# Performance work log

Measured on AMD Instinct MI355X. Metric: run time of the kernel, lower is better.

The kernel has to match this reference:

```python
import jax, jax.numpy as jnp
import numpy as np

B, N, F_IN, F_OUT = 4, 512, 128, 128


def setup_inputs() -> dict:
    key = jax.random.key(0)
    k_x, k_adj, k_wm, k_wu = jax.random.split(key, 4)
    x = jax.random.normal(k_x, (B, N, F_IN), dtype=jnp.float32)
    # binary adjacency mask (dense), avg degree ~ 0.1*N
    adj = (jax.random.uniform(k_adj, (B, N, N)) < 0.1).astype(jnp.float32)
    # Linear weights stored as [in, out] (transpose of torch's [out, in])
    s_m = 1.0 / np.sqrt(2 * F_IN)
    s_u = 1.0 / np.sqrt(F_IN + F_OUT)
    W_msg = jax.random.uniform(k_wm, (2 * F_IN, F_OUT), minval=-s_m, maxval=s_m, dtype=jnp.float32)
    b_msg = jnp.zeros((F_OUT,), dtype=jnp.float32)
    W_upd = jax.random.uniform(k_wu, (F_IN + F_OUT, F_OUT), minval=-s_u, maxval=s_u, dtype=jnp.float32)
    b_upd = jnp.zeros((F_OUT,), dtype=jnp.float32)
    return {"x": x, "adj": adj, "W_msg": W_msg, "b_msg": b_msg,
            "W_upd": W_upd, "b_upd": b_upd}


def reference(x, adj, W_msg, b_msg, W_upd, b_upd):
    # Linear(cat(x_i, x_j)) == x_i @ W_i + x_j @ W_j + b  (exploit linearity to
    # avoid materializing the [B,N,N,2F] concat; math identical to torch module)
    F_in = x.shape[-1]
    Wi, Wj = W_msg[:F_in], W_msg[F_in:]
    xi = jnp.einsum('bnf,fo->bno', x, Wi)            # [B,N,out], i-term
    xj = jnp.einsum('bnf,fo->bno', x, Wj)            # [B,N,out], j-term
    # messages[b,i,j,:] = relu(xi[b,i] + xj[b,j] + b_msg); dropout is identity (eval)
    messages = jax.nn.relu(xi[:, :, None, :] + xj[:, None, :, :] + b_msg)
    # mask by adjacency and sum over j
    aggregated = jnp.einsum('bijo,bij->bio', messages, adj)  # [B,N,out]
    h_new = jnp.concatenate([x, aggregated], axis=-1)        # [B,N,F+out]
    out = jax.nn.relu(jnp.einsum('bnf,fo->bno', h_new, W_upd) + b_upd)
    return out
```

## Files before the change

kernel.cpp:

```cpp
#include <hip/hip_runtime.h>
#include <hip/hip_fp16.h>

constexpr int B_   = 4;
constexpr int N_   = 512;
constexpr int F    = 128;
constexpr int R1B  = 8;
constexpr int R2B  = 8;
constexpr int LSTW = 520;

__global__ __launch_bounds__(512, 2) void k_pre(
    const float* __restrict__ x,
    const float* __restrict__ adj,
    const float* __restrict__ Wmsg,
    const float* __restrict__ bmsg,
    const float* __restrict__ Wupd,
    float*  __restrict__ xi,
    __half* __restrict__ xjH,
    float*  __restrict__ xu,
    int*    __restrict__ lstG,
    int*    __restrict__ cntG)
{
    __shared__ __align__(16) float xs[R1B][F];
    __shared__ __align__(16) int   lst[R1B][LSTW];
    __shared__ int   cntp[R1B];
    __shared__ float ps[4][3 * R1B][F];

    const int t    = threadIdx.x;
    const int lane = t & 63;
    const int w    = t >> 6;
    const int q    = t >> 7;
    const int o    = t & 127;
    const int r0   = blockIdx.x * R1B;
    const int b    = r0 >> 9;
    const int i0   = r0 & (N_ - 1);
    const int PADJ = B_ * N_ - b * N_;

    if (blockIdx.x == 0 && t < F)
        xjH[(size_t)(B_ * N_) * F + t] = __float2half(-60000.f);

    for (int idx = t; idx < R1B * F; idx += 512)
        xs[idx >> 7][idx & 127] = x[(size_t)r0 * F + idx];

    {
        const float* arow = adj + ((size_t)b * N_ + i0 + w) * N_;
        float a[8];
        #pragma unroll
        for (int s = 0; s < 8; ++s) a[s] = arow[s * 64 + lane];
        int base = 0;
        #pragma unroll
        for (int s = 0; s < 8; ++s) {
            const unsigned long long m = __ballot(a[s] != 0.f);
            const int off = __popcll(m & ((1ull << lane) - 1ull));
            if (a[s] != 0.f) lst[w][base + off] = s * 64 + lane;
            base += __popcll(m);
        }
        const int np = (base + 7) & ~7;
        if (lane < np - base) lst[w][base + lane] = PADJ;
        if (lane == 0) cntp[w] = np;
    }
    __syncthreads();

    #pragma unroll
    for (int r = 0; r < R1B; ++r)
        for (int k = t; k < cntp[r]; k += 512)
            lstG[(size_t)(r0 + r) * LSTW + k] = lst[r][k];
    if (t < R1B) cntG[r0 + t] = cntp[t];

    float ai[R1B] = {0,0,0,0,0,0,0,0};
    float aj[R1B] = {0,0,0,0,0,0,0,0};
    float au[R1B] = {0,0,0,0,0,0,0,0};
    const int kb = q * 32;
    #pragma unroll
    for (int k = 0; k < 32; k += 4) {
        float4 xv[R1B];
        #pragma unroll
        for (int r = 0; r < R1B; ++r)
            xv[r] = *reinterpret_cast<const float4*>(&xs[r][kb + k]);
        #pragma unroll
        for (int u = 0; u < 4; ++u) {
            const int kk = kb + k + u;
            const float wi = Wmsg[(size_t)kk * F + o];
            const float wj = Wmsg[(size_t)(F + kk) * F + o];
            const float wu = Wupd[(size_t)kk * F + o];
            #pragma unroll
            for (int r = 0; r < R1B; ++r) {
                const float xk = reinterpret_cast<const float*>(&xv[r])[u];
                ai[r] = fmaf(xk, wi, ai[r]);
                aj[r] = fmaf(xk, wj, aj[r]);
                au[r] = fmaf(xk, wu, au[r]);
            }
        }
    }
    #pragma unroll
    for (int r = 0; r < R1B; ++r) {
        ps[q][r][o]           = ai[r];
        ps[q][R1B + r][o]     = aj[r];
        ps[q][2 * R1B + r][o] = au[r];
    }
    __syncthreads();

    const float bm = bmsg[o];
    #pragma unroll
    for (int i = 0; i < 6; ++i) {
        const int v = q * 6 + i;
        const int r = v & (R1B - 1);
        const float s = ps[0][v][o] + ps[1][v][o] + ps[2][v][o] + ps[3][v][o];
        if (v < R1B)            xi[(size_t)(r0 + r) * F + o] = s + bm;
        else if (v < 2 * R1B)   xjH[(size_t)(r0 + r) * F + o] = __float2half(s);
        else                    xu[(size_t)(r0 + r) * F + o] = s;
    }
}

__global__ __launch_bounds__(512) void k_agg(
    const int*    __restrict__ lstG,
    const int*    __restrict__ cntG,
    const float*  __restrict__ xi,
    const __half* __restrict__ xjH,
    const float*  __restrict__ xu,
    const float*  __restrict__ Wupd,
    const float*  __restrict__ bupd,
    float* __restrict__ out)
{
    __shared__ __align__(16) float agg[R2B][F];

    const int t    = threadIdx.x;
    const int lane = t & 63;
    const int w    = t >> 6;
    const int o    = t & 127;
    const int gg   = t >> 7;
    const int r0   = blockIdx.x * R2B;
    const int b    = r0 >> 9;

    {
        const __half* xjb = xjH + (size_t)b * N_ * F;
        const float2 xir2 = *reinterpret_cast<const float2*>(
            &xi[(size_t)(r0 + w) * F + 2 * lane]);
        const int np = cntG[r0 + w];
        const int* lrow = lstG + (size_t)(r0 + w) * LSTW;
        float2 acc = {0.f, 0.f};

        if (np > 0) {
            int4 a = *reinterpret_cast<const int4*>(&lrow[0]);
            int4 c = *reinterpret_cast<const int4*>(&lrow[4]);
            for (int k = 0; k < np; k += 8) {
                const int4 an = *reinterpret_cast<const int4*>(&lrow[k + 8]);
                const int4 cn = *reinterpret_cast<const int4*>(&lrow[k + 12]);
                const float2 v0 = __half22float2(*reinterpret_cast<const __half2*>(&xjb[(size_t)a.x * F + 2 * lane]));
                const float2 v1 = __half22float2(*reinterpret_cast<const __half2*>(&xjb[(size_t)a.y * F + 2 * lane]));
                const float2 v2 = __half22float2(*reinterpret_cast<const __half2*>(&xjb[(size_t)a.z * F + 2 * lane]));
                const float2 v3 = __half22float2(*reinterpret_cast<const __half2*>(&xjb[(size_t)a.w * F + 2 * lane]));
                const float2 v4 = __half22float2(*reinterpret_cast<const __half2*>(&xjb[(size_t)c.x * F + 2 * lane]));
                const float2 v5 = __half22float2(*reinterpret_cast<const __half2*>(&xjb[(size_t)c.y * F + 2 * lane]));
                const float2 v6 = __half22float2(*reinterpret_cast<const __half2*>(&xjb[(size_t)c.z * F + 2 * lane]));
                const float2 v7 = __half22float2(*reinterpret_cast<const __half2*>(&xjb[(size_t)c.w * F + 2 * lane]));
                acc.x += fmaxf(xir2.x + v0.x, 0.f);  acc.y += fmaxf(xir2.y + v0.y, 0.f);
                acc.x += fmaxf(xir2.x + v1.x, 0.f);  acc.y += fmaxf(xir2.y + v1.y, 0.f);
                acc.x += fmaxf(xir2.x + v2.x, 0.f);  acc.y += fmaxf(xir2.y + v2.y, 0.f);
                acc.x += fmaxf(xir2.x + v3.x, 0.f);  acc.y += fmaxf(xir2.y + v3.y, 0.f);
                acc.x += fmaxf(xir2.x + v4.x, 0.f);  acc.y += fmaxf(xir2.y + v4.y, 0.f);
                acc.x += fmaxf(xir2.x + v5.x, 0.f);  acc.y += fmaxf(xir2.y + v5.y, 0.f);
                acc.x += fmaxf(xir2.x + v6.x, 0.f);  acc.y += fmaxf(xir2.y + v6.y, 0.f);
                acc.x += fmaxf(xir2.x + v7.x, 0.f);  acc.y += fmaxf(xir2.y + v7.y, 0.f);
                a = an; c = cn;
            }
        }
        *reinterpret_cast<float2*>(&agg[w][2 * lane]) = acc;
    }
    __syncthreads();

    float res0 = 0.f, res1 = 0.f;
    const int rA = 2 * gg, rB = 2 * gg + 1;
    #pragma unroll
    for (int k = 0; k < F; k += 4) {
        const float4 a0 = *reinterpret_cast<const float4*>(&agg[rA][k]);
        const float4 a1 = *reinterpret_cast<const float4*>(&agg[rB][k]);
        #pragma unroll
        for (int u = 0; u < 4; ++u) {
            const float wv = Wupd[(size_t)(F + k + u) * F + o];
            res0 = fmaf(reinterpret_cast<const float*>(&a0)[u], wv, res0);
            res1 = fmaf(reinterpret_cast<const float*>(&a1)[u], wv, res1);
        }
    }
    const float bu = bupd[o];
    out[(size_t)(r0 + rA) * F + o] =
        fmaxf(res0 + xu[(size_t)(r0 + rA) * F + o] + bu, 0.f);
    out[(size_t)(r0 + rB) * F + o] =
        fmaxf(res1 + xu[(size_t)(r0 + rB) * F + o] + bu, 0.f);
}

extern "C" void kernel_launch(void* const* d_in, const int* in_sizes, int n_in,
                              void* d_out, int out_size, void* d_ws, size_t ws_size,
                              hipStream_t stream)
{
    const float* x    = (const float*)d_in[0];
    const float* adj  = (const float*)d_in[1];
    const float* Wmsg = (const float*)d_in[2];
    const float* bmsg = (const float*)d_in[3];
    const float* Wupd = (const float*)d_in[4];
    const float* bupd = (const float*)d_in[5];
    float* out = (float*)d_out;

    const size_t rows = (size_t)B_ * N_;
    float*  xi   = (float*)d_ws;
    float*  xu   = xi + rows * F;
    int*    lstG = (int*)(xu + rows * F);
    int*    cntG = lstG + rows * LSTW;
    __half* xjH  = (__half*)(cntG + rows);

    k_pre<<<dim3(rows / R1B), dim3(512), 0, stream>>>(
        x, adj, Wmsg, bmsg, Wupd, xi, xjH, xu, lstG, cntG);
    k_agg<<<dim3(rows / R2B), dim3(512), 0, stream>>>(
        lstG, cntG, xi, xjH, xu, Wupd, bupd, out);
}
```

Before: 22.11 us.

## Compute pre-projections with bf16 MFMA and write neighbor lists directly

The fp32 FMA projection in k_pre is replaced by bf16 MFMA 16x16x32 tiles. x is converted to bf16 in shared memory, and the weights are converted on the fly from global memory. The grid now uses 128-thread blocks, each covering 16 rows and a quarter of the 48 output column tiles, and adjacency compaction writes straight to global memory instead of staging through LDS. This cuts FMA instruction count and LDS use and raises block count, but bf16 rounding of x and the weights lowers precision, and the weight loads are strided and repeated across blocks.

```diff
diff --git a/kernel.cpp b/kernel.cpp
--- a/kernel.cpp
+++ b/kernel.cpp
@@ -4,11 +4,20 @@
 constexpr int B_   = 4;
 constexpr int N_   = 512;
 constexpr int F    = 128;
-constexpr int R1B  = 8;
 constexpr int R2B  = 8;
 constexpr int LSTW = 520;
-
-__global__ __launch_bounds__(512, 2) void k_pre(
+constexpr int XPAD = 136;
+
+typedef short bf16x8 __attribute__((ext_vector_type(8)));
+typedef float f32x4  __attribute__((ext_vector_type(4)));
+
+__device__ inline ushort f2bf(float f) {
+    union { float f; uint u; } v; v.f = f;
+    const uint b = v.u + (0x7FFFu + ((v.u >> 16) & 1u));
+    return (ushort)(b >> 16);
+}
+
+__global__ __launch_bounds__(128) void k_pre(
     const float* __restrict__ x,
     const float* __restrict__ adj,
     const float* __restrict__ Wmsg,
@@ -20,94 +29,95 @@
     int*    __restrict__ lstG,
     int*    __restrict__ cntG)
 {
-    __shared__ __align__(16) float xs[R1B][F];
-    __shared__ __align__(16) int   lst[R1B][LSTW];
-    __shared__ int   cntp[R1B];
-    __shared__ float ps[4][3 * R1B][F];
+    __shared__ __align__(16) ushort xsb[16][XPAD];
 
     const int t    = threadIdx.x;
     const int lane = t & 63;
-    const int w    = t >> 6;
-    const int q    = t >> 7;
-    const int o    = t & 127;
-    const int r0   = blockIdx.x * R1B;
+    const int wv   = t >> 6;
+    const int mt   = blockIdx.x >> 2;
+    const int nq   = blockIdx.x & 3;
+    const int r0   = mt * 16;
     const int b    = r0 >> 9;
     const int i0   = r0 & (N_ - 1);
     const int PADJ = B_ * N_ - b * N_;
 
-    if (blockIdx.x == 0 && t < F)
-        xjH[(size_t)(B_ * N_) * F + t] = __float2half(-60000.f);
-
-    for (int idx = t; idx < R1B * F; idx += 512)
-        xs[idx >> 7][idx & 127] = x[(size_t)r0 * F + idx];
+    if (blockIdx.x == 0) xjH[(size_t)(B_ * N_) * F + t] = __float2half(-60000.f);
 
     {
-        const float* arow = adj + ((size_t)b * N_ + i0 + w) * N_;
-        float a[8];
-        #pragma unroll
-        for (int s = 0; s < 8; ++s) a[s] = arow[s * 64 + lane];
+        const int row = t >> 3, c16 = (t & 7) * 16;
+        const float* src = &x[(size_t)(r0 + row) * F + c16];
+        #pragma unroll
+        for (int hh = 0; hh < 2; ++hh) {
+            const float4 p0 = *reinterpret_cast<const float4*>(src + hh * 8);
+            const float4 p1 = *reinterpret_cast<const float4*>(src + hh * 8 + 4);
+            uint4 pk;
+            pk.x = (uint)f2bf(p0.x) | ((uint)f2bf(p0.y) << 16);
+            pk.y = (uint)f2bf(p0.z) | ((uint)f2bf(p0.w) << 16);
+            pk.z = (uint)f2bf(p1.x) | ((uint)f2bf(p1.y) << 16);
+            pk.w = (uint)f2bf(p1.z) | ((uint)f2bf(p1.w) << 16);
+            *reinterpret_cast<uint4*>(&xsb[row][c16 + hh * 8]) = pk;
+        }
+    }
+
+    #pragma unroll
+    for (int p = 0; p < 2; ++p) {
+        const int lr = nq * 4 + wv * 2 + p;
+        const float* arow = adj + (size_t)(b * N_ + i0 + lr) * N_;
+        int* lrow = lstG + (size_t)(r0 + lr) * LSTW;
         int base = 0;
         #pragma unroll
         for (int s = 0; s < 8; ++s) {
-            const unsigned long long m = __ballot(a[s] != 0.f);
+            const float a = arow[s * 64 + lane];
+            const unsigned long long m = __ballot(a != 0.f);
             const int off = __popcll(m & ((1ull << lane) - 1ull));
-            if (a[s] != 0.f) lst[w][base + off] = s * 64 + lane;
+            if (a != 0.f) lrow[base + off] = s * 64 + lane;
             base += __popcll(m);
         }
         const int np = (base + 7) & ~7;
-        if (lane < np - base) lst[w][base + lane] = PADJ;
-        if (lane == 0) cntp[w] = np;
+        if (lane < np - base) lrow[base + lane] = PADJ;
+        if (lane == 0) cntG[r0 + lr] = np;
     }
     __syncthreads();
 
-    #pragma unroll
-    for (int r = 0; r < R1B; ++r)
-        for (int k = t; k < cntp[r]; k += 512)
-            lstG[(size_t)(r0 + r) * LSTW + k] = lst[r][k];
-    if (t < R1B) cntG[r0 + t] = cntp[t];
-
-    float ai[R1B] = {0,0,0,0,0,0,0,0};
-    float aj[R1B] = {0,0,0,0,0,0,0,0};
-    float au[R1B] = {0,0,0,0,0,0,0,0};
-    const int kb = q * 32;
-    #pragma unroll
-    for (int k = 0; k < 32; k += 4) {
-        float4 xv[R1B];
-        #pragma unroll
-        for (int r = 0; r < R1B; ++r)
-            xv[r] = *reinterpret_cast<const float4*>(&xs[r][kb + k]);
-        #pragma unroll
-        for (int u = 0; u < 4; ++u) {
-            const int kk = kb + k + u;
-            const float wi = Wmsg[(size_t)kk * F + o];
-            const float wj = Wmsg[(size_t)(F + kk) * F + o];
-            const float wu = Wupd[(size_t)kk * F + o];
-            #pragma unroll
-            for (int r = 0; r < R1B; ++r) {
-                const float xk = reinterpret_cast<const float*>(&xv[r])[u];
-                ai[r] = fmaf(xk, wi, ai[r]);
-                aj[r] = fmaf(xk, wj, aj[r]);
-                au[r] = fmaf(xk, wu, au[r]);
-            }
-        }
-    }
-    #pragma unroll
-    for (int r = 0; r < R1B; ++r) {
-        ps[q][r][o]           = ai[r];
-        ps[q][R1B + r][o]     = aj[r];
-        ps[q][2 * R1B + r][o] = au[r];
-    }
-    __syncthreads();
-
-    const float bm = bmsg[o];
-    #pragma unroll
-    for (int i = 0; i < 6; ++i) {
-        const int v = q * 6 + i;
-        const int r = v & (R1B - 1);
-        const float s = ps[0][v][o] + ps[1][v][o] + ps[2][v][o] + ps[3][v][o];
-        if (v < R1B)            xi[(size_t)(r0 + r) * F + o] = s + bm;
-        else if (v < 2 * R1B)   xjH[(size_t)(r0 + r) * F + o] = __float2half(s);
-        else                    xu[(size_t)(r0 + r) * F + o] = s;
+    const int arow = lane & 15, kg = lane >> 4;
+    bf16x8 afr[4];
+    #pragma unroll
+    for (int ks = 0; ks < 4; ++ks)
+        afr[ks] = *reinterpret_cast<const bf16x8*>(&xsb[arow][ks * 32 + kg * 8]);
+
+    const int col = lane & 15;
+    #pragma unroll
+    for (int j = 0; j < 3; ++j) {
+        const int nt = nq * 6 + wv * 3 + j;
+        const int o  = (nt & 7) * 16 + col;
+        const float* wsrc = (nt < 8) ? Wmsg
+                          : (nt < 16) ? (Wmsg + (size_t)F * F)
+                          : Wupd;
+        f32x4 acc = {0.f, 0.f, 0.f, 0.f};
+        #pragma unroll
+        for (int ks = 0; ks < 4; ++ks) {
+            const int k0 = ks * 32 + kg * 8;
+            bf16x8 bfr;
+            #pragma unroll
+            for (int e = 0; e < 8; ++e)
+                bfr[e] = (short)f2bf(wsrc[(size_t)(k0 + e) * F + o]);
+            acc = __builtin_amdgcn_mfma_f32_16x16x32_bf16(afr[ks], bfr, acc, 0, 0, 0);
+        }
+        const int orow = r0 + (lane >> 4) * 4;
+        if (nt < 8) {
+            const float bm = bmsg[o];
+            #pragma unroll
+            for (int g = 0; g < 4; ++g)
+                xi[(size_t)(orow + g) * F + o] = acc[g] + bm;
+        } else if (nt < 16) {
+            #pragma unroll
+            for (int g = 0; g < 4; ++g)
+                xjH[(size_t)(orow + g) * F + o] = __float2half(acc[g]);
+        } else {
+            #pragma unroll
+            for (int g = 0; g < 4; ++g)
+                xu[(size_t)(orow + g) * F + o] = acc[g];
+        }
     }
 }
 
@@ -207,7 +217,7 @@
     int*    cntG = lstG + rows * LSTW;
     __half* xjH  = (__half*)(cntG + rows);
 
-    k_pre<<<dim3(rows / R1B), dim3(512), 0, stream>>>(
+    k_pre<<<dim3((rows / 16) * 4), dim3(128), 0, stream>>>(
         x, adj, Wmsg, bmsg, Wupd, xi, xjH, xu, lstG, cntG);
     k_agg<<<dim3(rows / R2B), dim3(512), 0, stream>>>(
         lstG, cntG, xi, xjH, xu, Wupd, bupd, out);
```

Result: slower. 23.65 us (+7.0%).
